# Kernel tuning notes

Hardware: AMD Instinct MI355X
Metric: run time of the kernel (lower is better)

Reference implementation:

```python
import jax, jax.numpy as jnp
import numpy as np
import math

B, S, D = 16, 512, 512
H = 8
RET = 512  # return_dim, multiple of D
EPS = 1e-12


def _xavier(key, shape):
    bound = math.sqrt(6.0 / (shape[0] + shape[1]))
    return jax.random.uniform(key, shape, jnp.float32, -bound, bound)


def setup_inputs() -> dict:
    key = jax.random.key(0)
    ks = jax.random.split(key, 7)
    x = jax.random.normal(ks[0], (B, S, D), jnp.float32)
    WQ = _xavier(ks[1], (D, D))
    WK = _xavier(ks[2], (D, D))
    WV = _xavier(ks[3], (D, D))
    # LazyLinear over flattened (S*D) features; stored [in, out] for clean matmul
    Wlin = jax.random.normal(ks[4], (S * D, RET), jnp.float32) / math.sqrt(S * D)
    blin = jnp.zeros((RET,), jnp.float32)
    ln_w = jnp.ones((D,), jnp.float32)
    ln_b = jnp.zeros((D,), jnp.float32)
    return {"x": x, "WQ": WQ, "WK": WK, "WV": WV,
            "Wlin": Wlin, "blin": blin, "ln_w": ln_w, "ln_b": ln_b}


def _swish(v):
    return v * jax.nn.sigmoid(v)


def reference(x, WQ, WK, WV, Wlin, blin, ln_w, ln_b):
    b, s, d = x.shape
    dh = d // H
    # QKV projections -> [b, h, s, dh]
    Q = (x @ WQ).reshape(b, s, H, dh).transpose(0, 2, 1, 3)
    K = (x @ WK).reshape(b, s, H, dh).transpose(0, 2, 1, 3)
    V = (x @ WV).reshape(b, s, H, dh).transpose(0, 2, 1, 3)
    # swish-gated attention scores (no softmax)
    scores = jnp.einsum('bhqd,bhkd->bhqk', Q, K) / math.sqrt(dh)
    scores = _swish(scores)
    out = jnp.einsum('bhqk,bhkd->bqhd', scores, V).reshape(b, s, d)
    # residual + TF-style LayerNorm (residual_coef = 1)
    out = out + x
    u = out.mean(-1, keepdims=True)
    var = jnp.mean((out - u) ** 2, axis=-1, keepdims=True)
    out = ln_w * ((out - u) / jnp.sqrt(var + EPS)) + ln_b
    # linear over flattened seq*d features, swish, reshape (dropout = identity, eval)
    y = out.reshape(b, -1) @ Wlin + blin
    y = _swish(y)
    return y.reshape(b, -1, d)
```

## Files before the change

kernel.cpp:

```cpp
#include <hip/hip_runtime.h>
#include <cstdint>

#define TB 16
#define TS 512
#define TD 512
#define TH 8
#define TDH 64
#define TSD (TS*TD)

typedef __attribute__((ext_vector_type(8))) short s16x8;
typedef __attribute__((ext_vector_type(4))) float f32x4;
typedef unsigned short bfu;

__device__ __forceinline__ unsigned short f2b(float f) {
  unsigned int u = __float_as_uint(f);
  u += 0x7FFFu + ((u >> 16) & 1u);
  return (unsigned short)(u >> 16);
}
__device__ __forceinline__ float b2f(bfu h) {
  return __uint_as_float(((unsigned)h) << 16);
}

__device__ __forceinline__ void gll16(const void* g, void* l) {
  __builtin_amdgcn_global_load_lds((const __attribute__((address_space(1))) void*)g,
                                   (__attribute__((address_space(3))) void*)l, 16, 0, 0);
}

__device__ __forceinline__ f32x4 MFMA16(s16x8 a, s16x8 b, f32x4 c) {
  return __builtin_amdgcn_mfma_f32_16x16x32_bf16(a, b, c, 0, 0, 0);
}

__global__ __launch_bounds__(256) void k_cast_x(const float4* __restrict__ x, ushort4* __restrict__ xb) {
  int i = blockIdx.x * 256 + threadIdx.x;
  float4 v = x[i];
  ushort4 o; o.x = f2b(v.x); o.y = f2b(v.y); o.z = f2b(v.z); o.w = f2b(v.w);
  xb[i] = o;
}

__global__ __launch_bounds__(256) void k_prep_w(const float* __restrict__ WQ, const float* __restrict__ WK,
                                                const float* __restrict__ WV, bfu* __restrict__ wt) {
  __shared__ float tile[64][65];
  int bk = blockIdx.x & 7;
  int bn = blockIdx.x >> 3;
  const float* W = bn < 8 ? WQ : (bn < 16 ? WK : WV);
  int ncol0 = (bn & 7) * 64;
  int t = threadIdx.x, tx = t & 63, ty = t >> 6;
  #pragma unroll
  for (int i = 0; i < 16; ++i) {
    int kl = i * 4 + ty;
    tile[kl][tx] = W[(size_t)(bk * 64 + kl) * 512 + ncol0 + tx];
  }
  __syncthreads();
  #pragma unroll
  for (int i = 0; i < 16; ++i) {
    int nl = i * 4 + ty;
    wt[(size_t)(bn * 64 + nl) * 512 + bk * 64 + tx] = f2b(tile[tx][nl]);
  }
}

__global__ __launch_bounds__(256) void k_qkv(const bfu* __restrict__ xb, const bfu* __restrict__ wt,
                                             bfu* __restrict__ qb, bfu* __restrict__ kb, bfu* __restrict__ vtb) {
  __shared__ __align__(16) bfu At[128 * 32];
  __shared__ __align__(16) bfu Bt[128 * 32];
  int t = threadIdx.x, lane = t & 63, w = t >> 6;
  int wr = w >> 1, wc = w & 1;
  int m0 = blockIdx.x * 128, n0 = blockIdx.y * 128;
  int fr = lane & 15, hi = lane >> 4;
  f32x4 acc[4][4] = {};
  for (int k0 = 0; k0 < TD; k0 += 32) {
    #pragma unroll
    for (int i = 0; i < 2; ++i) {
      int base = (i * 4 + w) * 1024;
      int seg  = (i * 4 + w) * 64 + lane;
      int row = seg >> 2, cs = seg & 3;
      gll16(xb + (size_t)(m0 + row) * TD + k0 + cs * 8, (char*)At + base);
      gll16(wt + (size_t)(n0 + row) * TD + k0 + cs * 8, (char*)Bt + base);
    }
    __syncthreads();
    s16x8 a[4], bb[4];
    #pragma unroll
    for (int m = 0; m < 4; ++m) a[m]  = *(const s16x8*)&At[(wr * 64 + m * 16 + fr) * 32 + hi * 8];
    #pragma unroll
    for (int n = 0; n < 4; ++n) bb[n] = *(const s16x8*)&Bt[(wc * 64 + n * 16 + fr) * 32 + hi * 8];
    #pragma unroll
    for (int m = 0; m < 4; ++m)
      #pragma unroll
      for (int n = 0; n < 4; ++n)
        acc[m][n] = MFMA16(a[m], bb[n], acc[m][n]);
    __syncthreads();
  }
  #pragma unroll
  for (int m = 0; m < 4; ++m) {
    int grow = m0 + wr * 64 + m * 16 + hi * 4;
    #pragma unroll
    for (int n = 0; n < 4; ++n) {
      int gcol = n0 + wc * 64 + n * 16 + fr;
      if (gcol < 512) {
        #pragma unroll
        for (int r = 0; r < 4; ++r) qb[(size_t)(grow + r) * TD + gcol] = f2b(acc[m][n][r]);
      } else if (gcol < 1024) {
        int c = gcol - 512;
        #pragma unroll
        for (int r = 0; r < 4; ++r) kb[(size_t)(grow + r) * TD + c] = f2b(acc[m][n][r]);
      } else {
        int c = gcol - 1024;
        int hh = c >> 6, dc = c & 63;
        int b_ = grow >> 9, s = grow & 511;
        ushort4 pk;
        pk.x = f2b(acc[m][n][0]); pk.y = f2b(acc[m][n][1]);
        pk.z = f2b(acc[m][n][2]); pk.w = f2b(acc[m][n][3]);
        *(ushort4*)&vtb[((size_t)((b_ * TH + hh) * TDH + dc) << 9) + s] = pk;
      }
    }
  }
}

__global__ __launch_bounds__(256) void k_attn(const bfu* __restrict__ qb, const bfu* __restrict__ kb,
                                              const bfu* __restrict__ vtb, const bfu* __restrict__ xb,
                                              float* __restrict__ ao) {
  __shared__ __align__(16) bfu Qs[64 * 72];
  __shared__ __align__(16) bfu Ks[128 * 72];
  __shared__ __align__(16) bfu Vs[64 * 136];
  __shared__ __align__(16) bfu Ps[64 * 136];
  int t = threadIdx.x, lane = t & 63, w = t >> 6;
  int qt = blockIdx.x, h = blockIdx.y, b = blockIdx.z;
  size_t qrow0 = (size_t)b * TS + qt * 64;
  int fr = lane & 15, hi = lane >> 4;
  #pragma unroll
  for (int i = 0; i < 2; ++i) {
    int seg = i * 256 + t, row = seg >> 3, cs = seg & 7;
    s16x8 v = *(const s16x8*)(qb + (qrow0 + row) * TD + h * TDH + cs * 8);
    *(s16x8*)&Qs[row * 72 + cs * 8] = v;
  }
  f32x4 acc_o[4] = {};
  for (int kt = 0; kt < 4; ++kt) {
    #pragma unroll
    for (int i = 0; i < 4; ++i) {
      int seg = i * 256 + t, row = seg >> 3, cs = seg & 7;
      s16x8 v = *(const s16x8*)(kb + ((size_t)b * TS + kt * 128 + row) * TD + h * TDH + cs * 8);
      *(s16x8*)&Ks[row * 72 + cs * 8] = v;
    }
    #pragma unroll
    for (int i = 0; i < 4; ++i) {
      int seg = i * 256 + t, row = seg >> 4, cs = seg & 15;
      s16x8 v = *(const s16x8*)(vtb + ((size_t)(b * TH + h) * TDH + row) * TS + kt * 128 + cs * 8);
      *(s16x8*)&Vs[row * 136 + cs * 8] = v;
    }
    __syncthreads();
    s16x8 aq0 = *(const s16x8*)&Qs[(w * 16 + fr) * 72 + hi * 8];
    s16x8 aq1 = *(const s16x8*)&Qs[(w * 16 + fr) * 72 + 32 + hi * 8];
    f32x4 sc[8];
    #pragma unroll
    for (int kj = 0; kj < 8; ++kj) {
      s16x8 b0 = *(const s16x8*)&Ks[(kj * 16 + fr) * 72 + hi * 8];
      s16x8 b1 = *(const s16x8*)&Ks[(kj * 16 + fr) * 72 + 32 + hi * 8];
      f32x4 c = {};
      c = MFMA16(aq0, b0, c);
      c = MFMA16(aq1, b1, c);
      sc[kj] = c;
    }
    #pragma unroll
    for (int kj = 0; kj < 8; ++kj) {
      #pragma unroll
      for (int r = 0; r < 4; ++r) {
        float v = sc[kj][r] * 0.125f;
        float p = v / (1.f + __expf(-v));
        Ps[(w * 16 + hi * 4 + r) * 136 + kj * 16 + fr] = f2b(p);
      }
    }
    __syncthreads();
    #pragma unroll
    for (int ks = 0; ks < 4; ++ks) {
      s16x8 pa = *(const s16x8*)&Ps[(w * 16 + fr) * 136 + ks * 32 + hi * 8];
      #pragma unroll
      for (int dn = 0; dn < 4; ++dn) {
        s16x8 vb = *(const s16x8*)&Vs[(dn * 16 + fr) * 136 + ks * 32 + hi * 8];
        acc_o[dn] = MFMA16(pa, vb, acc_o[dn]);
      }
    }
    __syncthreads();
  }
  #pragma unroll
  for (int dn = 0; dn < 4; ++dn) {
    int col = h * TDH + dn * 16 + fr;
    #pragma unroll
    for (int r = 0; r < 4; ++r) {
      size_t row = qrow0 + w * 16 + hi * 4 + r;
      ao[row * TD + col] = acc_o[dn][r] + b2f(xb[row * TD + col]);
    }
  }
}

__global__ __launch_bounds__(256) void k_ln(const float* __restrict__ a, const float* __restrict__ w,
                                            const float* __restrict__ bias, bfu* __restrict__ o) {
  int row = blockIdx.x, t = threadIdx.x;
  float2 v = *(const float2*)(a + (size_t)row * TD + t * 2);
  float s = v.x + v.y;
  #pragma unroll
  for (int off = 32; off > 0; off >>= 1) s += __shfl_down(s, off);
  __shared__ float r1[4], r2[4];
  int lane = t & 63, wv = t >> 6;
  if (lane == 0) r1[wv] = s;
  __syncthreads();
  float mean = (r1[0] + r1[1] + r1[2] + r1[3]) * (1.f / TD);
  float dx = v.x - mean, dy = v.y - mean;
  float q = dx * dx + dy * dy;
  #pragma unroll
  for (int off = 32; off > 0; off >>= 1) q += __shfl_down(q, off);
  if (lane == 0) r2[wv] = q;
  __syncthreads();
  float var = (r2[0] + r2[1] + r2[2] + r2[3]) * (1.f / TD);
  float inv = rsqrtf(var + 1e-12f);
  float2 wv2 = *(const float2*)(w + t * 2);
  float2 bv2 = *(const float2*)(bias + t * 2);
  unsigned pack = (unsigned)f2b(wv2.x * dx * inv + bv2.x) |
                  ((unsigned)f2b(wv2.y * dy * inv + bv2.y) << 16);
  *(unsigned*)(o + (size_t)row * TD + t * 2) = pack;
}

__global__ __launch_bounds__(256) void k_lin_part(const bfu* __restrict__ ln, const float* __restrict__ wl,
                                                  float* __restrict__ part) {
  __shared__ float al[512 * 20];
  int t = threadIdx.x;
  int kc = blockIdx.x >> 1;
  int ch = blockIdx.x & 1;
  int k0 = kc * 512;
  #pragma unroll
  for (int m = 0; m < 16; ++m) {
    al[t * 20 + m]         = b2f(ln[(size_t)m * TSD + k0 + t]);
    al[(256 + t) * 20 + m] = b2f(ln[(size_t)m * TSD + k0 + 256 + t]);
  }
  __syncthreads();
  float acc[16] = {};
  const float* wp = wl + (size_t)k0 * 512 + ch * 256 + t;
  #pragma unroll 8
  for (int k = 0; k < 512; ++k) {
    float wv = __builtin_nontemporal_load(wp + (size_t)k * 512);
    const float* ar = &al[k * 20];
    float4 a0 = *(const float4*)(ar);
    float4 a1 = *(const float4*)(ar + 4);
    float4 a2 = *(const float4*)(ar + 8);
    float4 a3 = *(const float4*)(ar + 12);
    acc[0]  += a0.x * wv; acc[1]  += a0.y * wv; acc[2]  += a0.z * wv; acc[3]  += a0.w * wv;
    acc[4]  += a1.x * wv; acc[5]  += a1.y * wv; acc[6]  += a1.z * wv; acc[7]  += a1.w * wv;
    acc[8]  += a2.x * wv; acc[9]  += a2.y * wv; acc[10] += a2.z * wv; acc[11] += a2.w * wv;
    acc[12] += a3.x * wv; acc[13] += a3.y * wv; acc[14] += a3.z * wv; acc[15] += a3.w * wv;
  }
  #pragma unroll
  for (int m = 0; m < 16; ++m)
    part[(size_t)kc * 8192 + m * 512 + ch * 256 + t] = acc[m];
}

__global__ __launch_bounds__(256) void k_lin_red1(const float* __restrict__ part, float* __restrict__ part2) {
  int t = threadIdx.x;
  int cs = blockIdx.x >> 5;
  int ob = blockIdx.x & 31;
  int o = ob * 256 + t;
  float s = 0.f;
  #pragma unroll 8
  for (int c = cs * 64; c < cs * 64 + 64; ++c) s += part[(size_t)c * 8192 + o];
  part2[(size_t)cs * 8192 + o] = s;
}

__global__ __launch_bounds__(256) void k_lin_red2(const float* __restrict__ part2, const float* __restrict__ blin,
                                                  float* __restrict__ out) {
  int o = blockIdx.x * 256 + threadIdx.x;
  float s = 0.f;
  #pragma unroll
  for (int c = 0; c < 8; ++c) s += part2[(size_t)c * 8192 + o];
  float v = s + blin[o & 511];
  out[o] = v / (1.f + __expf(-v));
}

extern "C" void kernel_launch(void* const* d_in, const int* in_sizes, int n_in,
                              void* d_out, int out_size, void* d_ws, size_t ws_size,
                              hipStream_t stream) {
  const float* x   = (const float*)d_in[0];
  const float* WQ  = (const float*)d_in[1];
  const float* WK  = (const float*)d_in[2];
  const float* WV  = (const float*)d_in[3];
  const float* Wl  = (const float*)d_in[4];
  const float* bl  = (const float*)d_in[5];
  const float* lnw = (const float*)d_in[6];
  const float* lnb = (const float*)d_in[7];
  float* out = (float*)d_out;
  char* ws = (char*)d_ws;
  bfu* xb  = (bfu*)ws;
  bfu* wt  = xb + 4194304;
  bfu* qb  = wt + 786432;
  bfu* kb  = qb + 4194304;
  bfu* vtb = kb + 4194304;
  float* attn  = (float*)(vtb + 4194304);
  bfu*   lno   = (bfu*)(attn + 4194304);
  float* part  = (float*)(lno + 4194304);
  float* part2 = part + 4194304;

  k_cast_x  <<<4096, 256, 0, stream>>>((const float4*)x, (ushort4*)xb);
  k_prep_w  <<<192, 256, 0, stream>>>(WQ, WK, WV, wt);
  k_qkv     <<<dim3(64, 12), 256, 0, stream>>>(xb, wt, qb, kb, vtb);
  k_attn    <<<dim3(8, 8, 16), 256, 0, stream>>>(qb, kb, vtb, xb, attn);
  k_ln      <<<8192, 256, 0, stream>>>(attn, lnw, lnb, lno);
  k_lin_part<<<1024, 256, 0, stream>>>(lno, Wl, part);
  k_lin_red1<<<256, 256, 0, stream>>>(part, part2);
  k_lin_red2<<<32, 256, 0, stream>>>(part2, bl, out);
}
```

Baseline: 214.6 us.

## Fuse LayerNorm into linear partial kernel and drop attention barrier

Removes the standalone LayerNorm kernel and its bf16 intermediate buffer. LayerNorm is now computed per row inside the linear partial-sum kernel, with 16-lane shuffle reductions, and written straight into shared memory in fp32. The change also deletes a __syncthreads between the score write and the P·V read in attention, which relies on each wave reading only its own rows of Ps. It also raises an unroll factor in the first reduction. Each LN row is computed twice, once per output-half block, which adds some redundant work while saving a kernel launch and a round trip through global memory.

```diff
diff --git a/kernel.cpp b/kernel.cpp
--- a/kernel.cpp
+++ b/kernel.cpp
@@ -168,7 +168,6 @@
         Ps[(w * 16 + hi * 4 + r) * 136 + kj * 16 + fr] = f2b(p);
       }
     }
-    __syncthreads();
     #pragma unroll
     for (int ks = 0; ks < 4; ++ks) {
       s16x8 pa = *(const s16x8*)&Ps[(w * 16 + fr) * 136 + ks * 32 + hi * 8];
@@ -191,44 +190,46 @@
   }
 }
 
-__global__ __launch_bounds__(256) void k_ln(const float* __restrict__ a, const float* __restrict__ w,
-                                            const float* __restrict__ bias, bfu* __restrict__ o) {
-  int row = blockIdx.x, t = threadIdx.x;
-  float2 v = *(const float2*)(a + (size_t)row * TD + t * 2);
-  float s = v.x + v.y;
-  #pragma unroll
-  for (int off = 32; off > 0; off >>= 1) s += __shfl_down(s, off);
-  __shared__ float r1[4], r2[4];
-  int lane = t & 63, wv = t >> 6;
-  if (lane == 0) r1[wv] = s;
-  __syncthreads();
-  float mean = (r1[0] + r1[1] + r1[2] + r1[3]) * (1.f / TD);
-  float dx = v.x - mean, dy = v.y - mean;
-  float q = dx * dx + dy * dy;
-  #pragma unroll
-  for (int off = 32; off > 0; off >>= 1) q += __shfl_down(q, off);
-  if (lane == 0) r2[wv] = q;
-  __syncthreads();
-  float var = (r2[0] + r2[1] + r2[2] + r2[3]) * (1.f / TD);
-  float inv = rsqrtf(var + 1e-12f);
-  float2 wv2 = *(const float2*)(w + t * 2);
-  float2 bv2 = *(const float2*)(bias + t * 2);
-  unsigned pack = (unsigned)f2b(wv2.x * dx * inv + bv2.x) |
-                  ((unsigned)f2b(wv2.y * dy * inv + bv2.y) << 16);
-  *(unsigned*)(o + (size_t)row * TD + t * 2) = pack;
-}
-
-__global__ __launch_bounds__(256) void k_lin_part(const bfu* __restrict__ ln, const float* __restrict__ wl,
+__global__ __launch_bounds__(256) void k_lin_part(const float* __restrict__ attn, const float* __restrict__ lnw,
+                                                  const float* __restrict__ lnb, const float* __restrict__ wl,
                                                   float* __restrict__ part) {
   __shared__ float al[512 * 20];
   int t = threadIdx.x;
   int kc = blockIdx.x >> 1;
   int ch = blockIdx.x & 1;
   int k0 = kc * 512;
-  #pragma unroll
-  for (int m = 0; m < 16; ++m) {
-    al[t * 20 + m]         = b2f(ln[(size_t)m * TSD + k0 + t]);
-    al[(256 + t) * 20 + m] = b2f(ln[(size_t)m * TSD + k0 + 256 + t]);
+  {
+    int m = t >> 4, d0 = (t & 15) * 32;
+    const float* row = attn + ((size_t)m * TS + kc) * TD;
+    float4 v[8];
+    float s = 0.f;
+    #pragma unroll
+    for (int j = 0; j < 8; ++j) {
+      v[j] = *(const float4*)(row + d0 + j * 4);
+      s += v[j].x + v[j].y + v[j].z + v[j].w;
+    }
+    #pragma unroll
+    for (int off = 8; off > 0; off >>= 1) s += __shfl_xor(s, off, 16);
+    float mean = s * (1.f / 512.f);
+    float q = 0.f;
+    #pragma unroll
+    for (int j = 0; j < 8; ++j) {
+      float dx = v[j].x - mean, dy = v[j].y - mean, dz = v[j].z - mean, dw = v[j].w - mean;
+      q += dx * dx + dy * dy + dz * dz + dw * dw;
+    }
+    #pragma unroll
+    for (int off = 8; off > 0; off >>= 1) q += __shfl_xor(q, off, 16);
+    float inv = rsqrtf(q * (1.f / 512.f) + 1e-12f);
+    #pragma unroll
+    for (int j = 0; j < 8; ++j) {
+      float4 wv = *(const float4*)(lnw + d0 + j * 4);
+      float4 bv = *(const float4*)(lnb + d0 + j * 4);
+      int d = d0 + j * 4;
+      al[(d + 0) * 20 + m] = wv.x * (v[j].x - mean) * inv + bv.x;
+      al[(d + 1) * 20 + m] = wv.y * (v[j].y - mean) * inv + bv.y;
+      al[(d + 2) * 20 + m] = wv.z * (v[j].z - mean) * inv + bv.z;
+      al[(d + 3) * 20 + m] = wv.w * (v[j].w - mean) * inv + bv.w;
+    }
   }
   __syncthreads();
   float acc[16] = {};
@@ -257,7 +258,7 @@
   int ob = blockIdx.x & 31;
   int o = ob * 256 + t;
   float s = 0.f;
-  #pragma unroll 8
+  #pragma unroll 16
   for (int c = cs * 64; c < cs * 64 + 64; ++c) s += part[(size_t)c * 8192 + o];
   part2[(size_t)cs * 8192 + o] = s;
 }
@@ -291,16 +292,14 @@
   bfu* kb  = qb + 4194304;
   bfu* vtb = kb + 4194304;
   float* attn  = (float*)(vtb + 4194304);
-  bfu*   lno   = (bfu*)(attn + 4194304);
-  float* part  = (float*)(lno + 4194304);
+  float* part  = attn + 4194304;
   float* part2 = part + 4194304;
 
   k_cast_x  <<<4096, 256, 0, stream>>>((const float4*)x, (ushort4*)xb);
   k_prep_w  <<<192, 256, 0, stream>>>(WQ, WK, WV, wt);
   k_qkv     <<<dim3(64, 12), 256, 0, stream>>>(xb, wt, qb, kb, vtb);
   k_attn    <<<dim3(8, 8, 16), 256, 0, stream>>>(qb, kb, vtb, xb, attn);
-  k_ln      <<<8192, 256, 0, stream>>>(attn, lnw, lnb, lno);
-  k_lin_part<<<1024, 256, 0, stream>>>(lno, Wl, part);
+  k_lin_part<<<1024, 256, 0, stream>>>(attn, lnw, lnb, Wl, part);
   k_lin_red1<<<256, 256, 0, stream>>>(part, part2);
   k_lin_red2<<<32, 256, 0, stream>>>(part2, bl, out);
 }
```

After: 212.4 us. No clear change (-1.0%).
